# Optimization experiments

Hardware: AMD Instinct MI355X
Metric: run time of the kernel (lower is better)

## Reference

```python
import jax, jax.numpy as jnp
import numpy as np
import math

COV_WEIGHT = 1.0
BANDWIDTH_FACTOR = 1.06
SQRT_2PI = math.sqrt(2.0 * math.pi)
EPS_LOG = 1e-8
H_MIN = 1e-4


def setup_inputs() -> dict:
    key = jax.random.key(0)
    activity = jax.random.normal(key, (2048, 64), dtype=jnp.float32)
    return {"activity": activity}


def reference(activity):
    B, R = activity.shape
    # Silverman bandwidth per receptor (torch .std uses ddof=1)
    std = jnp.std(activity, axis=0, ddof=1)                     # (R,)
    h = jnp.maximum(BANDWIDTH_FACTOR * std * (B ** (-0.2)), H_MIN)  # (R,)

    # Pairwise Gaussian KDE: query == samples == activity
    u = (activity[:, None, :] - activity[None, :, :]) / h       # (B_q, B_s, R)
    kernel_values = jnp.exp(-0.5 * u * u) / SQRT_2PI             # (B_q, B_s, R)
    density = kernel_values.sum(axis=1) / (B * h)                # (B_q, R)

    entropies = -jnp.mean(jnp.log(density + EPS_LOG), axis=0)    # (R,)
    loss_entropy = -entropies.mean()

    # Covariance penalty: sum of squared off-diagonals
    centered = activity - activity.mean(axis=0, keepdims=True)
    cov = (centered.T @ centered) / (B - 1)                      # (R, R)
    off = cov - jnp.diag(jnp.diag(cov))
    loss_cov = jnp.sum(off * off)

    total_loss = loss_entropy + COV_WEIGHT * loss_cov
    return total_loss
```

## Files before the change

kernel.cpp:

```cpp
#include <hip/hip_runtime.h>
#include <math.h>

#define B_SZ 2048
#define R_SZ 64
#define QT 4
#define KDE_BLOCKS (B_SZ / QT)

#define B_POW_NEG02 0.217637640824031f
#define SQRT_2PI 2.5066282746310002f
#define LOG2E 1.44269504088896340736f

extern "C" __device__ float __ocml_native_exp2_f32(float);

typedef __attribute__((ext_vector_type(2))) float f32x2;


__global__ __launch_bounds__(1024) void stats_gram_kernel(const float* __restrict__ A,
                                                          float* __restrict__ qsums,
                                                          float* __restrict__ qsums2,
                                                          float* __restrict__ gram4,
                                                          float* __restrict__ ent_acc,
                                                          int* __restrict__ done_cnt) {
    int b = blockIdx.x;
    int i = b >> 2, qd = b & 3;
    int tid = threadIdx.x;
    int j = tid & 63, bg = tid >> 6;

    const float* __restrict__ Aq = A + (qd * 512) * R_SZ;
    float g = 0.f, sj = 0.f, s2j = 0.f;
#pragma unroll 4
    for (int t = bg; t < 512; t += 16) {
        float ai = Aq[t * R_SZ + i];
        float aj = Aq[t * R_SZ + j];
        g = fmaf(ai, aj, g);
        sj += aj;
        s2j = fmaf(aj, aj, s2j);
    }

    __shared__ float gred[16][64], sred[16][64], s2red[16][64];
    gred[bg][j] = g; sred[bg][j] = sj; s2red[bg][j] = s2j;
    __syncthreads();
    if (tid < 64) {
        float G = 0.f, S = 0.f, S2 = 0.f;
#pragma unroll
        for (int t = 0; t < 16; ++t) { G += gred[t][j]; S += sred[t][j]; S2 += s2red[t][j]; }
        gram4[b * 64 + j] = G;
        if (i == 0) {
            qsums[qd * 64 + j]  = S;
            qsums2[qd * 64 + j] = S2;
        }
    }
    if (b == 0 && tid == 64) { *ent_acc = 0.f; *done_cnt = 0; }
}

__global__ __launch_bounds__(1024) void kde_kernel(const float* __restrict__ A,
                                                   const float* __restrict__ qsums,
                                                   const float* __restrict__ qsums2,
                                                   const float* __restrict__ gram4,
                                                   float* __restrict__ ent_acc,
                                                   int* __restrict__ done_cnt,
                                                   float* __restrict__ out) {
    int tid = threadIdx.x;
    int r = tid & 63, sg = tid >> 6;

    __shared__ float k0s[64], lscs[64], sums_s[64];
    if (tid < 64) {
        float S  = qsums[tid]  + qsums[64 + tid]  + qsums[128 + tid]  + qsums[192 + tid];
        float S2 = qsums2[tid] + qsums2[64 + tid] + qsums2[128 + tid] + qsums2[192 + tid];
        float m = S * (1.f / (float)B_SZ);
        float var = (S2 - S * m) * (1.f / (float)(B_SZ - 1));
        var = fmaxf(var, 0.f);
        float h = fmaxf(1.06f * sqrtf(var) * B_POW_NEG02, 1e-4f);
        k0s[tid]  = sqrtf(0.5f * LOG2E) / h;
        lscs[tid] = 1.0f / ((float)B_SZ * h * SQRT_2PI);
        sums_s[tid] = S;
    }
    __syncthreads();
    float k0 = k0s[r];

    int q0 = blockIdx.x * QT;
    f32x2 uq01 = { A[(q0 + 0) * R_SZ + r] * k0, A[(q0 + 1) * R_SZ + r] * k0 };
    f32x2 uq23 = { A[(q0 + 2) * R_SZ + r] * k0, A[(q0 + 3) * R_SZ + r] * k0 };
    f32x2 c01 = { 0.f, 0.f }, c23 = { 0.f, 0.f };

#define KDE_BODY(usv)                                                          \
    {                                                                          \
        f32x2 uss = { (usv), (usv) };                                          \
        f32x2 d01 = uq01 - uss, d23 = uq23 - uss;                              \
        f32x2 n01 = -d01 * d01, n23 = -d23 * d23;                              \
        f32x2 e01 = { __ocml_native_exp2_f32(n01.x), __ocml_native_exp2_f32(n01.y) }; \
        f32x2 e23 = { __ocml_native_exp2_f32(n23.x), __ocml_native_exp2_f32(n23.y) }; \
        c01 += e01; c23 += e23;                                                \
    }

    const float* __restrict__ Ap = A + sg * R_SZ + r;
    float p[8];
#pragma unroll
    for (int j = 0; j < 8; ++j) p[j] = Ap[j * 1024];

    int li = 8 * 1024;
#pragma unroll 1
    for (int k = 0; k < 15; ++k) {
#pragma unroll
        for (int j = 0; j < 8; ++j) {
            float us = p[j] * k0;
            p[j] = Ap[li + j * 1024];
            KDE_BODY(us);
        }
        li += 8 * 1024;
    }
#pragma unroll
    for (int j = 0; j < 8; ++j) { float us = p[j] * k0; KDE_BODY(us); }

#undef KDE_BODY

    __shared__ float red[16][QT][64];
    red[sg][0][r] = c01.x; red[sg][1][r] = c01.y;
    red[sg][2][r] = c23.x; red[sg][3][r] = c23.y;
    __syncthreads();
    __shared__ float wred[QT];
    if (sg < QT) {
        float S = 0.f;
#pragma unroll
        for (int t = 0; t < 16; ++t) S += red[t][sg][r];
        float v = __logf(fmaf(S, lscs[r], 1e-8f));
        for (int off = 32; off > 0; off >>= 1) v += __shfl_down(v, off, 64);
        if (r == 0) wred[sg] = v;
    }
    __syncthreads();
    __shared__ int lastflag;
    if (tid == 0) {
        float p2 = 0.f;
#pragma unroll
        for (int t = 0; t < QT; ++t) p2 += wred[t];
        p2 *= (1.0f / ((float)B_SZ * (float)R_SZ));
        atomicAdd(ent_acc, p2);
        __threadfence();
        int prev = atomicAdd(done_cnt, 1);
        lastflag = (prev == KDE_BLOCKS - 1);
    }
    __syncthreads();
    if (lastflag) {
        __threadfence();
        float v = 0.f;
#pragma unroll
        for (int c = tid; c < 4096; c += 1024) {
            int ii = c >> 6, jj = c & 63;
            const float* gp = gram4 + ii * 256 + jj;
            float G = gp[0] + gp[64] + gp[128] + gp[192];
            float mi = sums_s[ii] * (1.f / (float)B_SZ);
            float mj = sums_s[jj] * (1.f / (float)B_SZ);
            float cov = (G - (float)B_SZ * mi * mj) * (1.f / (float)(B_SZ - 1));
            if (ii != jj) v = fmaf(cov, cov, v);
        }
        for (int off = 32; off > 0; off >>= 1) v += __shfl_down(v, off, 64);
        __shared__ float wsum[16];
        if (r == 0) wsum[sg] = v;
        __syncthreads();
        if (tid == 0) {
            float C = 0.f;
#pragma unroll
            for (int t = 0; t < 16; ++t) C += wsum[t];
            float ent = __hip_atomic_load(ent_acc, __ATOMIC_ACQUIRE,
                                          __HIP_MEMORY_SCOPE_AGENT);
            out[0] = ent + C;
        }
    }
}

extern "C" void kernel_launch(void* const* d_in, const int* in_sizes, int n_in,
                              void* d_out, int out_size, void* d_ws, size_t ws_size,
                              hipStream_t stream) {
    const float* A = (const float*)d_in[0];
    float* out = (float*)d_out;

    float* wsf = (float*)d_ws;
    float* qsums   = wsf;
    float* qsums2  = wsf + 256;
    float* ent_acc = wsf + 640;
    int*   done_cnt = (int*)(wsf + 672);
    float* gram4   = wsf + 1024;

    stats_gram_kernel<<<256, 1024, 0, stream>>>(A, qsums, qsums2, gram4,
                                                ent_acc, done_cnt);
    kde_kernel<<<KDE_BLOCKS, 1024, 0, stream>>>(A, qsums, qsums2, gram4,
                                                ent_acc, done_cnt, out);
}
```

Measured before the change: 100.1 us.

## Exploit KDE pairwise symmetry with triangular tile scheduling and atomic density accumulation

Splits the pairwise KDE into upper-triangular 64x64 tile pairs so each symmetric kernel value is computed once and credited to both query and sample rows. Off-diagonal contributions to the sample side are accumulated through LDS atomics and then added to a global density buffer, with a new finish kernel computing the log-density entropy and covariance penalty. This aims to roughly halve the exp work, at the cost of per-element LDS atomics, global atomics, buffer zeroing and an extra kernel launch.

```diff
diff --git a/kernel.cpp b/kernel.cpp
--- a/kernel.cpp
+++ b/kernel.cpp
@@ -3,8 +3,12 @@
 
 #define B_SZ 2048
 #define R_SZ 64
-#define QT 4
-#define KDE_BLOCKS (B_SZ / QT)
+#define NTILE 32
+#define TILE 64
+#define JW 32
+#define NOFF 496
+#define KDE_BLOCKS (64 + 2 * NOFF)
+#define FIN_BLOCKS 32
 
 #define B_POW_NEG02 0.217637640824031f
 #define SQRT_2PI 2.5066282746310002f
@@ -20,7 +24,8 @@
                                                           float* __restrict__ qsums2,
                                                           float* __restrict__ gram4,
                                                           float* __restrict__ ent_acc,
-                                                          int* __restrict__ done_cnt) {
+                                                          int* __restrict__ done2,
+                                                          float* __restrict__ dens) {
     int b = blockIdx.x;
     int i = b >> 2, qd = b & 3;
     int tid = threadIdx.x;
@@ -37,6 +42,8 @@
         s2j = fmaf(aj, aj, s2j);
     }
 
+    if (tid < 512) dens[b * 512 + tid] = 0.f;
+
     __shared__ float gred[16][64], sred[16][64], s2red[16][64];
     gred[bg][j] = g; sred[bg][j] = sj; s2red[bg][j] = s2j;
     __syncthreads();
@@ -50,20 +57,22 @@
             qsums2[qd * 64 + j] = S2;
         }
     }
-    if (b == 0 && tid == 64) { *ent_acc = 0.f; *done_cnt = 0; }
+    if (b == 0 && tid == 512) { *ent_acc = 0.f; *done2 = 0; }
 }
 
 __global__ __launch_bounds__(1024) void kde_kernel(const float* __restrict__ A,
                                                    const float* __restrict__ qsums,
                                                    const float* __restrict__ qsums2,
-                                                   const float* __restrict__ gram4,
-                                                   float* __restrict__ ent_acc,
-                                                   int* __restrict__ done_cnt,
-                                                   float* __restrict__ out) {
+                                                   float* __restrict__ dens) {
     int tid = threadIdx.x;
     int r = tid & 63, sg = tid >> 6;
 
-    __shared__ float k0s[64], lscs[64], sums_s[64];
+    __shared__ float k0s[64];
+    __shared__ float ldsJ[JW][64];
+
+    ((float*)ldsJ)[tid] = 0.f;
+    ((float*)ldsJ)[tid + 1024] = 0.f;
+
     if (tid < 64) {
         float S  = qsums[tid]  + qsums[64 + tid]  + qsums[128 + tid]  + qsums[192 + tid];
         float S2 = qsums2[tid] + qsums2[64 + tid] + qsums2[128 + tid] + qsums2[192 + tid];
@@ -71,19 +80,31 @@
         float var = (S2 - S * m) * (1.f / (float)(B_SZ - 1));
         var = fmaxf(var, 0.f);
         float h = fmaxf(1.06f * sqrtf(var) * B_POW_NEG02, 1e-4f);
-        k0s[tid]  = sqrtf(0.5f * LOG2E) / h;
-        lscs[tid] = 1.0f / ((float)B_SZ * h * SQRT_2PI);
-        sums_s[tid] = S;
+        k0s[tid] = sqrtf(0.5f * LOG2E) / h;
     }
     __syncthreads();
     float k0 = k0s[r];
 
-    int q0 = blockIdx.x * QT;
-    f32x2 uq01 = { A[(q0 + 0) * R_SZ + r] * k0, A[(q0 + 1) * R_SZ + r] * k0 };
-    f32x2 uq23 = { A[(q0 + 2) * R_SZ + r] * k0, A[(q0 + 3) * R_SZ + r] * k0 };
+    int a, bT, half, isoff;
+    {
+        int bid = blockIdx.x;
+        if (bid < 64) { a = bid >> 1; bT = a; half = bid & 1; isoff = 0; }
+        else {
+            int t = bid - 64; int p = t >> 1; half = t & 1; isoff = 1;
+            int len = NTILE - 1; a = 0;
+            while (p >= len && len > 0) { p -= len; --len; ++a; }
+            bT = a + 1 + p;
+        }
+    }
+    int Ibase = a * TILE;
+    int Jbase = bT * TILE + half * JW;
+
+    int i0 = Ibase + sg * 4;
+    f32x2 uq01 = { A[(i0 + 0) * R_SZ + r] * k0, A[(i0 + 1) * R_SZ + r] * k0 };
+    f32x2 uq23 = { A[(i0 + 2) * R_SZ + r] * k0, A[(i0 + 3) * R_SZ + r] * k0 };
     f32x2 c01 = { 0.f, 0.f }, c23 = { 0.f, 0.f };
 
-#define KDE_BODY(usv)                                                          \
+#define KDE_BODY(usv, jj)                                                      \
     {                                                                          \
         f32x2 uss = { (usv), (usv) };                                          \
         f32x2 d01 = uq01 - uss, d23 = uq23 - uss;                              \
@@ -91,58 +112,96 @@
         f32x2 e01 = { __ocml_native_exp2_f32(n01.x), __ocml_native_exp2_f32(n01.y) }; \
         f32x2 e23 = { __ocml_native_exp2_f32(n23.x), __ocml_native_exp2_f32(n23.y) }; \
         c01 += e01; c23 += e23;                                                \
-    }
-
-    const float* __restrict__ Ap = A + sg * R_SZ + r;
-    float p[8];
-#pragma unroll
-    for (int j = 0; j < 8; ++j) p[j] = Ap[j * 1024];
-
-    int li = 8 * 1024;
+        if (isoff) {                                                           \
+            float jp = (e01.x + e01.y) + (e23.x + e23.y);                      \
+            atomicAdd(&ldsJ[jj][r], jp);                       \
+        }                                                                      \
+    }
+
+    const float* __restrict__ Ap = A + Jbase * R_SZ + r;
+    float p[4];
+#pragma unroll
+    for (int j = 0; j < 4; ++j) p[j] = Ap[j * 64];
+
+    int li = 4 * 64, s = 0;
 #pragma unroll 1
-    for (int k = 0; k < 15; ++k) {
-#pragma unroll
-        for (int j = 0; j < 8; ++j) {
+    for (int k = 0; k < 7; ++k) {
+#pragma unroll
+        for (int j = 0; j < 4; ++j) {
             float us = p[j] * k0;
-            p[j] = Ap[li + j * 1024];
-            KDE_BODY(us);
-        }
-        li += 8 * 1024;
-    }
-#pragma unroll
-    for (int j = 0; j < 8; ++j) { float us = p[j] * k0; KDE_BODY(us); }
+            p[j] = Ap[li + j * 64];
+            KDE_BODY(us, s + j);
+        }
+        s += 4; li += 4 * 64;
+    }
+#pragma unroll
+    for (int j = 0; j < 4; ++j) { float us = p[j] * k0; KDE_BODY(us, s + j); }
 
 #undef KDE_BODY
 
-    __shared__ float red[16][QT][64];
-    red[sg][0][r] = c01.x; red[sg][1][r] = c01.y;
-    red[sg][2][r] = c23.x; red[sg][3][r] = c23.y;
-    __syncthreads();
-    __shared__ float wred[QT];
-    if (sg < QT) {
-        float S = 0.f;
-#pragma unroll
-        for (int t = 0; t < 16; ++t) S += red[t][sg][r];
-        float v = __logf(fmaf(S, lscs[r], 1e-8f));
-        for (int off = 32; off > 0; off >>= 1) v += __shfl_down(v, off, 64);
-        if (r == 0) wred[sg] = v;
-    }
-    __syncthreads();
+    atomicAdd(&dens[(i0 + 0) * R_SZ + r], c01.x);
+    atomicAdd(&dens[(i0 + 1) * R_SZ + r], c01.y);
+    atomicAdd(&dens[(i0 + 2) * R_SZ + r], c23.x);
+    atomicAdd(&dens[(i0 + 3) * R_SZ + r], c23.y);
+    __syncthreads();
+    if (isoff) {
+        int j1 = sg * 2, j2 = sg * 2 + 1;
+        atomicAdd(&dens[(Jbase + j1) * R_SZ + r], ldsJ[j1][r]);
+        atomicAdd(&dens[(Jbase + j2) * R_SZ + r], ldsJ[j2][r]);
+    }
+}
+
+__global__ __launch_bounds__(1024) void finish_kernel(const float* __restrict__ qsums,
+                                                      const float* __restrict__ qsums2,
+                                                      const float* __restrict__ gram4,
+                                                      const float* __restrict__ dens,
+                                                      float* __restrict__ ent_acc,
+                                                      int* __restrict__ done2,
+                                                      float* __restrict__ out) {
+    int tid = threadIdx.x;
+    int r = tid & 63, sg = tid >> 6;
+    int g = blockIdx.x;
+
+    __shared__ float lscs[64], sums_s[64];
+    __shared__ float wred[16];
+    if (tid < 64) {
+        float S  = qsums[tid]  + qsums[64 + tid]  + qsums[128 + tid]  + qsums[192 + tid];
+        float S2 = qsums2[tid] + qsums2[64 + tid] + qsums2[128 + tid] + qsums2[192 + tid];
+        float m = S * (1.f / (float)B_SZ);
+        float var = (S2 - S * m) * (1.f / (float)(B_SZ - 1));
+        var = fmaxf(var, 0.f);
+        float h = fmaxf(1.06f * sqrtf(var) * B_POW_NEG02, 1e-4f);
+        lscs[tid] = 1.0f / ((float)B_SZ * h * SQRT_2PI);
+        sums_s[tid] = S;
+    }
+    __syncthreads();
+
+    float v = 0.f;
+#pragma unroll
+    for (int m = 0; m < 4; ++m) {
+        int row = g * TILE + sg * 4 + m;
+        float S = dens[row * R_SZ + r];
+        v += __logf(fmaf(S, lscs[r], 1e-8f));
+    }
+    for (int off = 32; off > 0; off >>= 1) v += __shfl_down(v, off, 64);
+    if (r == 0) wred[sg] = v;
+    __syncthreads();
+
     __shared__ int lastflag;
     if (tid == 0) {
         float p2 = 0.f;
 #pragma unroll
-        for (int t = 0; t < QT; ++t) p2 += wred[t];
+        for (int t = 0; t < 16; ++t) p2 += wred[t];
         p2 *= (1.0f / ((float)B_SZ * (float)R_SZ));
         atomicAdd(ent_acc, p2);
         __threadfence();
-        int prev = atomicAdd(done_cnt, 1);
-        lastflag = (prev == KDE_BLOCKS - 1);
+        int prev = atomicAdd(done2, 1);
+        lastflag = (prev == FIN_BLOCKS - 1);
     }
     __syncthreads();
     if (lastflag) {
         __threadfence();
-        float v = 0.f;
+        float v2 = 0.f;
 #pragma unroll
         for (int c = tid; c < 4096; c += 1024) {
             int ii = c >> 6, jj = c & 63;
@@ -151,11 +210,11 @@
             float mi = sums_s[ii] * (1.f / (float)B_SZ);
             float mj = sums_s[jj] * (1.f / (float)B_SZ);
             float cov = (G - (float)B_SZ * mi * mj) * (1.f / (float)(B_SZ - 1));
-            if (ii != jj) v = fmaf(cov, cov, v);
-        }
-        for (int off = 32; off > 0; off >>= 1) v += __shfl_down(v, off, 64);
+            if (ii != jj) v2 = fmaf(cov, cov, v2);
+        }
+        for (int off = 32; off > 0; off >>= 1) v2 += __shfl_down(v2, off, 64);
         __shared__ float wsum[16];
-        if (r == 0) wsum[sg] = v;
+        if (r == 0) wsum[sg] = v2;
         __syncthreads();
         if (tid == 0) {
             float C = 0.f;
@@ -178,11 +237,13 @@
     float* qsums   = wsf;
     float* qsums2  = wsf + 256;
     float* ent_acc = wsf + 640;
-    int*   done_cnt = (int*)(wsf + 672);
+    int*   done2   = (int*)(wsf + 672);
     float* gram4   = wsf + 1024;
+    float* dens    = wsf + 20480;
 
     stats_gram_kernel<<<256, 1024, 0, stream>>>(A, qsums, qsums2, gram4,
-                                                ent_acc, done_cnt);
-    kde_kernel<<<KDE_BLOCKS, 1024, 0, stream>>>(A, qsums, qsums2, gram4,
-                                                ent_acc, done_cnt, out);
-}
+                                                ent_acc, done2, dens);
+    kde_kernel<<<KDE_BLOCKS, 1024, 0, stream>>>(A, qsums, qsums2, dens);
+    finish_kernel<<<FIN_BLOCKS, 1024, 0, stream>>>(qsums, qsums2, gram4, dens,
+                                                   ent_acc, done2, out);
+}
```

Result: slower. 236.3 us (+136.1%).
